# Kernel optimization log

Hardware: AMD Instinct MI355X
Metric: run time of the kernel (lower is better)

Reference implementation:

```python
import jax, jax.numpy as jnp
import numpy as np

B, S, D, H, DM, SS, A, HID = 2048, 64, 6, 4, 64, 150, 7, 256
FF = 4 * DM
DH = DM // H

def layernorm(x, g, b, eps=1e-5):
    m = jnp.mean(x, axis=-1, keepdims=True)
    v = jnp.mean((x - m) ** 2, axis=-1, keepdims=True)
    return (x - m) * jax.lax.rsqrt(v + eps) * g + b

def setup_inputs() -> dict:
    key = jax.random.key(0)
    ks = jax.random.split(key, 24)
    w = lambda k, sh: jax.random.normal(k, sh, dtype=jnp.float32) * 0.05
    inp = {
        'observation': jax.random.normal(ks[0], (B, SS), dtype=jnp.float32),
        'sequence': jax.random.normal(ks[1], (S, B, SS), dtype=jnp.float32),
        'memory': jax.random.normal(ks[2], (D, B, S, DM), dtype=jnp.float32) * 0.1,
        'length': jax.random.randint(ks[3], (1, B, 1), 0, S, dtype=jnp.int32),
        # input LayerNorm (state_size=150)
        'ln_g': jnp.ones((SS,), jnp.float32), 'ln_b': jnp.zeros((SS,), jnp.float32),
        # token_embedding replaced by Identity in source; embedding_dim(150)->dim(64) projection
        'W_emb': w(ks[4], (SS, DM)),
        # per-layer transformer params (stacked over depth)
        'ln1_g': jnp.ones((D, DM), jnp.float32), 'ln1_b': jnp.zeros((D, DM), jnp.float32),
        'ln2_g': jnp.ones((D, DM), jnp.float32), 'ln2_b': jnp.zeros((D, DM), jnp.float32),
        'Wq': w(ks[5], (D, DM, DM)), 'Wk': w(ks[6], (D, DM, DM)),
        'Wv': w(ks[7], (D, DM, DM)), 'Wo': w(ks[8], (D, DM, DM)),
        'W1': w(ks[9], (D, DM, FF)), 'b1': jnp.zeros((D, FF), jnp.float32),
        'W2': w(ks[10], (D, FF, DM)), 'b2': jnp.zeros((D, DM), jnp.float32),
        # policy MLP: dim -> 256 -> 2*action_size
        'Wp1': w(ks[11], (DM, HID)), 'bp1': jnp.zeros((HID,), jnp.float32),
        'Wp2': w(ks[12], (HID, 2 * A)), 'bp2': jnp.zeros((2 * A,), jnp.float32),
    }
    return inp

def reference(observation, sequence, memory, ln_g, ln_b, W_emb,
              ln1_g, ln1_b, ln2_g, ln2_b, Wq, Wk, Wv, Wo, W1, b1, W2, b2,
              Wp1, bp1, Wp2, bp2, length):
    # sample_forward (T == 1)
    obs = layernorm(observation, ln_g, ln_b)                      # (B,150)
    lidx = jnp.clip(length[0, :, 0], 0, S - 1)                    # (B,)
    bidx = jnp.arange(B)
    # index_put_: scatter current obs into sequence buffer at per-batch position
    seq = sequence.at[lidx, bidx].set(obs)                        # (S,B,150)
    x = jnp.einsum('bse,ed->bsd', seq.transpose(1, 0, 2), W_emb)  # (B,S,DM)
    # queries attend fully to the memory segment, causally within current segment
    causal = jnp.tril(jnp.ones((S, S), bool))
    mask = jnp.concatenate([jnp.ones((S, S), bool), causal], axis=1)  # (S, 2S)
    scale = 1.0 / np.sqrt(DH)
    new_mems = []
    for l in range(D):
        new_mems.append(x)                                        # hidden entering layer -> new memory
        h = layernorm(x, ln1_g[l], ln1_b[l])
        kv_in = jnp.concatenate([memory[l], h], axis=1)           # (B,2S,DM)
        q = (h @ Wq[l]).reshape(B, S, H, DH)
        k = (kv_in @ Wk[l]).reshape(B, 2 * S, H, DH)
        v = (kv_in @ Wv[l]).reshape(B, 2 * S, H, DH)
        scores = jnp.einsum('bqhd,bkhd->bhqk', q, k) * scale      # (B,H,S,2S)
        scores = jnp.where(mask[None, None], scores, jnp.finfo(scores.dtype).min)
        attn = jax.nn.softmax(scores, axis=-1)
        out = jnp.einsum('bhqk,bkhd->bqhd', attn, v).reshape(B, S, DM)
        x = x + out @ Wo[l]
        h2 = layernorm(x, ln2_g[l], ln2_b[l])
        x = x + jax.nn.relu(h2 @ W1[l] + b1[l]) @ W2[l] + b2[l]
    new_memory = jnp.stack(new_mems)                              # (D,B,S,DM)
    out_sb = x.transpose(1, 0, 2)                                 # (S,B,DM)
    output = out_sb[lidx, bidx]                                   # gather by length -> (B,DM)
    new_length = jnp.mod(length + 1, S)                           # (1,B,1)
    reset = (new_length[0, :, 0] == 0).astype(memory.dtype)[None, :, None, None]
    mem_out = reset * new_memory + (1.0 - reset) * memory         # masked memory reset/blend
    # policy head
    pol = jax.nn.relu(output @ Wp1 + bp1) @ Wp2 + bp2             # (B, 2A)
    std = jax.nn.softplus(pol[:, :A])
    mu = jnp.tanh(pol[:, A:])
    return (mu, std, seq, mem_out, new_length)
```

## Files before the change

kernel.cpp:

```cpp
#include <hip/hip_runtime.h>
#include <hip/hip_bf16.h>
#include <math.h>

#define NB 2048

#define LD4(p) (*(const float4*)(p))

#define O_STD 14336
#define O_SEQ 28672
#define O_MEM 19689472
#define O_LEN 70021120

#define WQT 0
#define WKT 24576
#define WVT 49152
#define WOT 73728
#define W1T 98304
#define W2T 196608
#define WET 294912

typedef __attribute__((ext_vector_type(8))) short short8v;
typedef __attribute__((ext_vector_type(4))) float f32x4;

#define MFMA(a, b, c) __builtin_amdgcn_mfma_f32_16x16x32_bf16((a), (b), (c), 0, 0, 0)

#define QSC 0.36067376022224087f

__device__ __forceinline__ short f2bf(float f) {
    return __builtin_bit_cast(short, (__bf16)f);
}
__device__ __forceinline__ unsigned pk2(float lo, float hi) {
    union { __hip_bfloat162 h; unsigned u; } t;
    t.h = __float22bfloat162_rn(make_float2(lo, hi));
    return t.u;
}

__global__ __launch_bounds__(256) void prep_weights(
        const float* __restrict__ Wq, const float* __restrict__ Wk,
        const float* __restrict__ Wv, const float* __restrict__ Wo,
        const float* __restrict__ W1, const float* __restrict__ W2,
        const float* __restrict__ Wemb, short* __restrict__ wsb) {
    int idx = blockIdx.x * 256 + threadIdx.x;
    {
        int l = idx >> 14, r = idx & 16383;
        { int n = r >> 6, k = r & 63;
          wsb[W1T + idx] = f2bf(W1[l * 16384 + k * 256 + n]); }
        { int n = r >> 8, k = r & 255;
          wsb[W2T + idx] = f2bf(W2[l * 16384 + k * 64 + n]); }
    }
    if (idx < 24576) {
        int l = idx >> 12, r = idx & 4095;
        int n = r >> 6, k = r & 63;
        int s = l * 4096 + k * 64 + n;
        wsb[WQT + idx] = f2bf(Wq[s]);
        wsb[WKT + idx] = f2bf(Wk[s]);
        wsb[WVT + idx] = f2bf(Wv[s]);
        wsb[WOT + idx] = f2bf(Wo[s]);
    }
    if (idx < 10240) {
        int n = idx / 160, k = idx - n * 160;
        wsb[WET + idx] = (k < 150) ? f2bf(Wemb[k * 64 + n]) : (short)0;
    }
}

__global__ __launch_bounds__(256) void copy4_kernel(const float4* __restrict__ src,
                                                    float4* __restrict__ dst, int n) {
    int i = blockIdx.x * 256 + threadIdx.x;
    if (i < n) dst[i] = src[i];
}

__global__ __launch_bounds__(256) void obs_ln_kernel(const float* __restrict__ obs,
        const float* __restrict__ g, const float* __restrict__ be,
        const int* __restrict__ len, float* __restrict__ outSeq, float* __restrict__ outLen) {
    int w = threadIdx.x >> 6, lane = threadIdx.x & 63;
    int b = blockIdx.x * 4 + w;
    const float* row = obs + (size_t)b * 150;
    float v0 = row[lane], v1 = row[64 + lane];
    float v2 = (lane < 22) ? row[128 + lane] : 0.f;
    float s = v0 + v1 + v2;
    #pragma unroll
    for (int m = 1; m <= 32; m <<= 1) s += __shfl_xor(s, m);
    float mean = s * (1.0f / 150.0f);
    float d0 = v0 - mean, d1 = v1 - mean;
    float d2 = (lane < 22) ? (v2 - mean) : 0.f;
    float q = d0 * d0 + d1 * d1 + d2 * d2;
    #pragma unroll
    for (int m = 1; m <= 32; m <<= 1) q += __shfl_xor(q, m);
    float rs = rsqrtf(q * (1.0f / 150.0f) + 1e-5f);
    int lenraw = len[b];
    int lidx = min(max(lenraw, 0), 63);
    float* orow = outSeq + ((size_t)lidx * NB + b) * 150;
    orow[lane]      = d0 * rs * g[lane] + be[lane];
    orow[64 + lane] = d1 * rs * g[64 + lane] + be[64 + lane];
    if (lane < 22) orow[128 + lane] = d2 * rs * g[128 + lane] + be[128 + lane];
    if (lane == 0) outLen[b] = (float)((lenraw + 1) & 63);
}

__global__ __launch_bounds__(256, 2) void mega_kernel(
        const float* __restrict__ seq, const float* __restrict__ memory,
        const int* __restrict__ len,
        const float* __restrict__ ln1g, const float* __restrict__ ln1b,
        const float* __restrict__ ln2g, const float* __restrict__ ln2b,
        const float* __restrict__ b1, const float* __restrict__ b2,
        const short* __restrict__ wsb,
        float* __restrict__ memOut, float* __restrict__ xrow) {
    __shared__ short L[20480];
    __shared__ float fls[576];
    float* lnp = fls;
    float* b1f = fls + 256;
    float* b2f = fls + 512;

    const int tid = threadIdx.x;
    const int b = blockIdx.x;
    const int w = tid >> 6;
    const int lane = tid & 63;
    const int g = lane >> 4;
    const int r16 = lane & 15;

    const int lenraw = len[b];
    const int lidx = min(max(lenraw, 0), 63);
    const bool reset = (((lenraw + 1) & 63) == 0);

    const int cxa = (r16 & 7) << 3;
    const int fc0 = (8 * g) ^ cxa;
    const int fc1 = (32 + 8 * g) ^ cxa;
    const int cxw = (g & 1) << 5;
    const int cxm = ((tid >> 2) & 7) << 3;

    const short8v zs = {0, 0, 0, 0, 0, 0, 0, 0};
    const f32x4 zf = {0.f, 0.f, 0.f, 0.f};

    #pragma unroll 1
    for (int j = 0; j < 16; ++j) {
        int r = w * 16 + j;
        int rb = r * 160;
        const float* srow = seq + ((size_t)r * NB + b) * 150;
        L[rb + lane]      = f2bf(srow[lane]);
        L[rb + 64 + lane] = f2bf(srow[64 + lane]);
        if (lane < 22)      L[rb + 128 + lane] = f2bf(srow[128 + lane]);
        else if (lane < 32) L[rb + 128 + lane] = 0;
    }
    {
        const int4* s4p = (const int4*)(wsb + WET);
        int4* d4p = (int4*)(L + 10240);
        #pragma unroll
        for (int i = 0; i < 5; ++i) d4p[tid + i * 256] = s4p[tid + i * 256];
    }
    __syncthreads();

    f32x4 x[4] = {zf, zf, zf, zf};
    #pragma unroll
    for (int kk = 0; kk < 5; ++kk) {
        short8v a = *(const short8v*)&L[(16 * w + r16) * 160 + kk * 32 + 8 * g];
        #pragma unroll
        for (int ct = 0; ct < 4; ++ct) {
            short8v bb = *(const short8v*)&L[10240 + (16 * ct + r16) * 160 + kk * 32 + 8 * g];
            x[ct] = MFMA(a, bb, x[ct]);
        }
    }
    __syncthreads();

    #pragma unroll 1
    for (int l = 0; l < 6; ++l) {
        if (tid < 64) {
            lnp[tid]       = ln1g[l * 64 + tid];
            lnp[64 + tid]  = ln1b[l * 64 + tid];
            lnp[128 + tid] = ln2g[l * 64 + tid];
            lnp[192 + tid] = ln2b[l * 64 + tid];
            b2f[tid]       = b2[l * 64 + tid];
        }
        b1f[tid] = b1[l * 256 + tid];
        {
            const float* gmem = memory + ((size_t)l * NB + b) * 4096;
            float* gout = memOut + ((size_t)l * NB + b) * 4096;
            int rr = tid >> 2, c0 = (tid & 3) * 16;
            #pragma unroll
            for (int k4 = 0; k4 < 4; ++k4) {
                float4 v = LD4(&gmem[rr * 64 + c0 + k4 * 4]);
                if (!reset) *(float4*)&gout[rr * 64 + c0 + k4 * 4] = v;
                uint2 su;
                su.x = pk2(v.x, v.y); su.y = pk2(v.z, v.w);
                *(uint2*)&L[rr * 64 + ((c0 + k4 * 4) ^ cxm)] = su;
            }
            if (reset) {
                #pragma unroll
                for (int ct = 0; ct < 4; ++ct)
                    #pragma unroll
                    for (int j = 0; j < 4; ++j)
                        gout[(16 * w + 4 * g + j) * 64 + 16 * ct + r16] = x[ct][j];
            }
        }
        {
            const int4* sq = (const int4*)(wsb + WQT + l * 4096);
            const int4* sk = (const int4*)(wsb + WKT + l * 4096);
            const int4* sv = (const int4*)(wsb + WVT + l * 4096);
            int4* dq = (int4*)(L + 8192);
            int4* dk = (int4*)(L + 12288);
            int4* dv = (int4*)(L + 16384);
            #pragma unroll
            for (int i = 0; i < 2; ++i) {
                int idx = tid + i * 256;
                int sx = idx ^ ((idx >> 3) & 7);
                dq[sx] = sq[idx];
                dk[sx] = sk[idx];
                dv[sx] = sv[idx];
            }
        }
        __syncthreads();

        #pragma unroll
        for (int j = 0; j < 4; ++j) {
            float s = x[0][j] + x[1][j] + x[2][j] + x[3][j];
            s += __shfl_xor(s, 1); s += __shfl_xor(s, 2);
            s += __shfl_xor(s, 4); s += __shfl_xor(s, 8);
            float m = s * 0.015625f;
            float q = 0.f;
            #pragma unroll
            for (int ct = 0; ct < 4; ++ct) { float d = x[ct][j] - m; q += d * d; }
            q += __shfl_xor(q, 1); q += __shfl_xor(q, 2);
            q += __shfl_xor(q, 4); q += __shfl_xor(q, 8);
            float rs = rsqrtf(q * 0.015625f + 1e-5f);
            #pragma unroll
            for (int ct = 0; ct < 4; ++ct) {
                int col = 16 * ct + r16;
                float hv = (x[ct][j] - m) * rs * lnp[col] + lnp[64 + col];
                L[(64 + 16 * w + 4 * g + j) * 64 + (col ^ (cxw | (j << 3)))] = f2bf(hv);
            }
        }
        __syncthreads();

        f32x4 qa[4] = {zf, zf, zf, zf};
        f32x4 ka[2][4] = {{zf, zf, zf, zf}, {zf, zf, zf, zf}};
        #pragma unroll
        for (int kk = 0; kk < 2; ++kk) {
            const int fc = kk ? fc1 : fc0;
            short8v ah = *(const short8v*)&L[(64 + 16 * w + r16) * 64 + fc];
            short8v a0 = *(const short8v*)&L[(16 * w + r16) * 64 + fc];
            #pragma unroll
            for (int ct = 0; ct < 4; ++ct) {
                short8v bq = *(const short8v*)&L[8192  + (16 * ct + r16) * 64 + fc];
                short8v bk = *(const short8v*)&L[12288 + (16 * ct + r16) * 64 + fc];
                qa[ct]    = MFMA(ah, bq, qa[ct]);
                ka[0][ct] = MFMA(a0, bk, ka[0][ct]);
                ka[1][ct] = MFMA(ah, bk, ka[1][ct]);
            }
        }
        __syncthreads();

        #pragma unroll
        for (int ct = 0; ct < 4; ++ct)
            #pragma unroll
            for (int j = 0; j < 4; ++j)
                L[8192 + (16 * w + 4 * g + j) * 64 + ((16 * ct + r16) ^ (cxw | (j << 3)))] =
                    f2bf(qa[ct][j] * QSC);

        f32x4 va[2][4] = {{zf, zf, zf, zf}, {zf, zf, zf, zf}};
        #pragma unroll
        for (int kk = 0; kk < 2; ++kk) {
            const int fc = kk ? fc1 : fc0;
            short8v ah = *(const short8v*)&L[(64 + 16 * w + r16) * 64 + fc];
            short8v a0 = *(const short8v*)&L[(16 * w + r16) * 64 + fc];
            #pragma unroll
            for (int ct = 0; ct < 4; ++ct) {
                short8v bv = *(const short8v*)&L[16384 + (16 * ct + r16) * 64 + fc];
                va[0][ct] = MFMA(a0, bv, va[0][ct]);
                va[1][ct] = MFMA(ah, bv, va[1][ct]);
            }
        }
        __syncthreads();

        #pragma unroll
        for (int ct = 0; ct < 4; ++ct) {
            #pragma unroll
            for (int j = 0; j < 4; ++j) {
                int key0 = 16 * w + 4 * g + j;
                int colw = (16 * ct + r16) ^ (cxw | (j << 3));
                L[key0 * 64 + colw] = f2bf(ka[0][ct][j]);
                L[(64 + key0) * 64 + colw] = f2bf(ka[1][ct][j]);
            }
        }
        {
            const int p0 = ((w >> 1) << 5) | (g << 3) | ((w & 1) << 2);
            const int p1 = p0 | 64;
            #pragma unroll
            for (int ct = 0; ct < 4; ++ct) {
                int rowb = 12288 + (16 * ct + r16) * 128;
                uint2 v0, v1;
                v0.x = pk2(va[0][ct][0], va[0][ct][1]);
                v0.y = pk2(va[0][ct][2], va[0][ct][3]);
                v1.x = pk2(va[1][ct][0], va[1][ct][1]);
                v1.y = pk2(va[1][ct][2], va[1][ct][3]);
                *(uint2*)&L[rowb + (p0 ^ cxa)] = v0;
                *(uint2*)&L[rowb + (p1 ^ cxa)] = v1;
            }
        }
        __syncthreads();

        const int hc = 16 * w;
        const int attc = (hc + 8 * g) ^ cxa;
        const int obc  = (hc + 4 * g) ^ cxa;
        #pragma unroll
        for (int qt = 0; qt < 4; ++qt) {
            const int KT = 5 + qt;
            short8v bQ = (g < 2) ? *(const short8v*)&L[8192 + (16 * qt + r16) * 64 + attc] : zs;
            f32x4 s[8];
            #pragma unroll
            for (int kt = 0; kt < 8; ++kt) if (kt < KT) {
                short8v aK = *(const short8v*)&L[(16 * kt + r16) * 64 + attc];
                s[kt] = MFMA(aK, bQ, zf);
            }
            float sum = 0.f;
            #pragma unroll
            for (int kt = 0; kt < 8; ++kt) if (kt < KT) {
                #pragma unroll
                for (int j = 0; j < 4; ++j) {
                    float e = exp2f(s[kt][j]);
                    if (kt == KT - 1) e = ((4 * g + j) > r16) ? 0.f : e;
                    s[kt][j] = e; sum += e;
                }
            }
            sum += __shfl_xor(sum, 16);
            sum += __shfl_xor(sum, 32);
            float inv = 1.0f / sum;
            f32x4 of = zf;
            const int KT2 = (KT + 1) >> 1;
            #pragma unroll
            for (int kt2 = 0; kt2 < 4; ++kt2) if (kt2 < KT2) {
                short8v aV = *(const short8v*)&L[12288 + (hc + r16) * 128 +
                                                 ((32 * kt2 + 8 * g) ^ cxa)];
                union { short8v v; unsigned u[4]; } pb;
                const int i0 = 2 * kt2, i1 = 2 * kt2 + 1;
                pb.u[0] = pk2(s[i0][0], s[i0][1]);
                pb.u[1] = pk2(s[i0][2], s[i0][3]);
                pb.u[2] = (i1 < KT) ? pk2(s[i1][0], s[i1][1]) : 0u;
                pb.u[3] = (i1 < KT) ? pk2(s[i1][2], s[i1][3]) : 0u;
                of = MFMA(aV, pb.v, of);
            }
            uint2 ov;
            ov.x = pk2(of[0] * inv, of[1] * inv);
            ov.y = pk2(of[2] * inv, of[3] * inv);
            *(uint2*)&L[8192 + (16 * qt + r16) * 64 + obc] = ov;
        }
        __syncthreads();

        {
            const int4* s = (const int4*)(wsb + WOT + l * 4096);
            int4* d = (int4*)(L + 0);
            #pragma unroll
            for (int i = 0; i < 2; ++i) {
                int idx = tid + i * 256;
                d[idx ^ ((idx >> 3) & 7)] = s[idx];
            }
        }
        __syncthreads();

        #pragma unroll
        for (int kk = 0; kk < 2; ++kk) {
            const int fc = kk ? fc1 : fc0;
            short8v a = *(const short8v*)&L[8192 + (16 * w + r16) * 64 + fc];
            #pragma unroll
            for (int ct = 0; ct < 4; ++ct) {
                short8v bb = *(const short8v*)&L[(16 * ct + r16) * 64 + fc];
                x[ct] = MFMA(a, bb, x[ct]);
            }
        }
        #pragma unroll
        for (int j = 0; j < 4; ++j) {
            float s = x[0][j] + x[1][j] + x[2][j] + x[3][j];
            s += __shfl_xor(s, 1); s += __shfl_xor(s, 2);
            s += __shfl_xor(s, 4); s += __shfl_xor(s, 8);
            float m = s * 0.015625f;
            float q = 0.f;
            #pragma unroll
            for (int ct = 0; ct < 4; ++ct) { float d = x[ct][j] - m; q += d * d; }
            q += __shfl_xor(q, 1); q += __shfl_xor(q, 2);
            q += __shfl_xor(q, 4); q += __shfl_xor(q, 8);
            float rs = rsqrtf(q * 0.015625f + 1e-5f);
            #pragma unroll
            for (int ct = 0; ct < 4; ++ct) {
                int col = 16 * ct + r16;
                float hv = (x[ct][j] - m) * rs * lnp[128 + col] + lnp[192 + col];
                L[4096 + (16 * w + 4 * g + j) * 64 + (col ^ (cxw | (j << 3)))] = f2bf(hv);
            }
        }
        __syncthreads();

        #pragma unroll 1
        for (int kb = 0; kb < 4; ++kb) {
            {
                const int4* s1 = (const int4*)(wsb + W1T + l * 16384 + kb * 4096);
                int4* d1 = (int4*)(L + 12288);
                int4* d2 = (int4*)(L + 8192);
                #pragma unroll
                for (int i = 0; i < 2; ++i) {
                    int idx = tid + i * 256;
                    int sx = idx ^ ((idx >> 3) & 7);
                    d1[sx] = s1[idx];
                    int n = idx >> 3, c = idx & 7;
                    d2[sx] = *(const int4*)&wsb[W2T + l * 16384 + n * 256 + kb * 64 + c * 8];
                }
            }
            __syncthreads();
            f32x4 tacc[4] = {zf, zf, zf, zf};
            #pragma unroll
            for (int kk = 0; kk < 2; ++kk) {
                const int fc = kk ? fc1 : fc0;
                short8v a = *(const short8v*)&L[4096 + (16 * w + r16) * 64 + fc];
                #pragma unroll
                for (int ct = 0; ct < 4; ++ct) {
                    short8v bb = *(const short8v*)&L[12288 + (16 * ct + r16) * 64 + fc];
                    tacc[ct] = MFMA(a, bb, tacc[ct]);
                }
            }
            #pragma unroll
            for (int ct = 0; ct < 4; ++ct)
                #pragma unroll
                for (int j = 0; j < 4; ++j) {
                    float v = fmaxf(tacc[ct][j] + b1f[kb * 64 + 16 * ct + r16], 0.f);
                    L[16384 + (16 * w + 4 * g + j) * 64 + ((16 * ct + r16) ^ (cxw | (j << 3)))] = f2bf(v);
                }
            __syncthreads();
            #pragma unroll
            for (int kk = 0; kk < 2; ++kk) {
                const int fc = kk ? fc1 : fc0;
                short8v a = *(const short8v*)&L[16384 + (16 * w + r16) * 64 + fc];
                #pragma unroll
                for (int ct = 0; ct < 4; ++ct) {
                    short8v bb = *(const short8v*)&L[8192 + (16 * ct + r16) * 64 + fc];
                    x[ct] = MFMA(a, bb, x[ct]);
                }
            }
            __syncthreads();
        }
        #pragma unroll
        for (int ct = 0; ct < 4; ++ct)
            #pragma unroll
            for (int j = 0; j < 4; ++j) x[ct][j] += b2f[16 * ct + r16];
    }

    if (w == (lidx >> 4) && g == ((lidx >> 2) & 3)) {
        int j = lidx & 3;
        #pragma unroll
        for (int ct = 0; ct < 4; ++ct) {
            float v = (j == 0) ? x[ct][0] : (j == 1) ? x[ct][1] : (j == 2) ? x[ct][2] : x[ct][3];
            xrow[(size_t)b * 64 + 16 * ct + r16] = v;
        }
    }
}

__device__ __forceinline__ float softplusf(float v) {
    return fmaxf(v, 0.f) + log1pf(expf(-fabsf(v)));
}

__global__ __launch_bounds__(256) void policy_kernel(const float* __restrict__ xrow,
        const float* __restrict__ Wp1, const float* __restrict__ bp1,
        const float* __restrict__ Wp2, const float* __restrict__ bp2,
        float* __restrict__ outMu, float* __restrict__ outStd) {
    __shared__ float sx[64];
    __shared__ float sh1[256];
    const int tid = threadIdx.x;
    for (int bi = 0; bi < 16; ++bi) {
        int b = blockIdx.x * 16 + bi;
        if (tid < 64) sx[tid] = xrow[(size_t)b * 64 + tid];
        __syncthreads();
        float acc = bp1[tid];
        #pragma unroll 16
        for (int k = 0; k < 64; ++k) acc = fmaf(sx[k], Wp1[k * 256 + tid], acc);
        sh1[tid] = fmaxf(acc, 0.f);
        __syncthreads();
        if (tid < 224) {
            int j = tid >> 4, gg = tid & 15;
            float a = 0.f;
            #pragma unroll
            for (int kk = 0; kk < 16; ++kk) {
                int k = gg * 16 + kk;
                a = fmaf(sh1[k], Wp2[k * 14 + j], a);
            }
            a += __shfl_xor(a, 1); a += __shfl_xor(a, 2);
            a += __shfl_xor(a, 4); a += __shfl_xor(a, 8);
            if (gg == 0) {
                float pol = a + bp2[j];
                if (j < 7) outStd[(size_t)b * 7 + j] = softplusf(pol);
                else       outMu[(size_t)b * 7 + (j - 7)] = tanhf(pol);
            }
        }
        __syncthreads();
    }
}

extern "C" void kernel_launch(void* const* d_in, const int* in_sizes, int n_in,
                              void* d_out, int out_size, void* d_ws, size_t ws_size,
                              hipStream_t stream) {
    const float* obs   = (const float*)d_in[0];
    const float* seqIn = (const float*)d_in[1];
    const float* mem   = (const float*)d_in[2];
    const int*   len   = (const int*)d_in[3];
    const float* ln_g  = (const float*)d_in[4];
    const float* ln_b  = (const float*)d_in[5];
    const float* Wemb  = (const float*)d_in[6];
    const float* ln1g  = (const float*)d_in[7];
    const float* ln1b  = (const float*)d_in[8];
    const float* ln2g  = (const float*)d_in[9];
    const float* ln2b  = (const float*)d_in[10];
    const float* Wq    = (const float*)d_in[11];
    const float* Wk    = (const float*)d_in[12];
    const float* Wv    = (const float*)d_in[13];
    const float* Wo    = (const float*)d_in[14];
    const float* W1    = (const float*)d_in[15];
    const float* b1    = (const float*)d_in[16];
    const float* W2    = (const float*)d_in[17];
    const float* b2    = (const float*)d_in[18];
    const float* Wp1   = (const float*)d_in[19];
    const float* bp1   = (const float*)d_in[20];
    const float* Wp2   = (const float*)d_in[21];
    const float* bp2   = (const float*)d_in[22];

    float* out    = (float*)d_out;
    float* outMu  = out;
    float* outStd = out + O_STD;
    float* outSeq = out + O_SEQ;
    float* outMem = out + O_MEM;
    float* outLen = out + O_LEN;
    float* xrow   = (float*)d_ws;
    short* wsb    = (short*)((char*)d_ws + 524288);

    hipLaunchKernelGGL(prep_weights, dim3(384), dim3(256), 0, stream,
                       Wq, Wk, Wv, Wo, W1, W2, Wemb, wsb);
    hipLaunchKernelGGL(copy4_kernel, dim3(19200), dim3(256), 0, stream,
                       (const float4*)seqIn, (float4*)outSeq, 4915200);
    hipLaunchKernelGGL(obs_ln_kernel, dim3(512), dim3(256), 0, stream,
                       obs, ln_g, ln_b, len, outSeq, outLen);
    hipLaunchKernelGGL(mega_kernel, dim3(2048), dim3(256), 0, stream,
                       outSeq, mem, len, ln1g, ln1b, ln2g, ln2b, b1, b2,
                       wsb, outMem, xrow);
    hipLaunchKernelGGL(policy_kernel, dim3(128), dim3(256), 0, stream,
                       xrow, Wp1, bp1, Wp2, bp2, outMu, outStd);
}
```

Baseline: 521.0 us.

## Re-plan LDS regions to prefetch Wo/W1/W2 and double-buffer FFN weight tiles

```diff
diff --git a/kernel.cpp b/kernel.cpp
--- a/kernel.cpp
+++ b/kernel.cpp
@@ -25,6 +25,14 @@
 #define MFMA(a, b, c) __builtin_amdgcn_mfma_f32_16x16x32_bf16((a), (b), (c), 0, 0, 0)
 
 #define QSC 0.36067376022224087f
+
+#define R_SKV   0
+#define R_A1    8192
+#define R_VT    12288
+#define R_WO    20480
+#define R_H2    24576
+#define R_W2B0  28672
+#define R_W2B1  32768
 
 __device__ __forceinline__ short f2bf(float f) {
     return __builtin_bit_cast(short, (__bf16)f);
@@ -104,7 +112,7 @@
         const float* __restrict__ b1, const float* __restrict__ b2,
         const short* __restrict__ wsb,
         float* __restrict__ memOut, float* __restrict__ xrow) {
-    __shared__ short L[20480];
+    __shared__ short L[36864];
     __shared__ float fls[576];
     float* lnp = fls;
     float* b1f = fls + 256;
@@ -162,6 +170,26 @@
 
     #pragma unroll 1
     for (int l = 0; l < 6; ++l) {
+        auto stage_sq = [&](const short* src, int dstbase) {
+            const int4* s = (const int4*)src;
+            int4* d = (int4*)(L + dstbase);
+            #pragma unroll
+            for (int i = 0; i < 2; ++i) {
+                int idx = tid + i * 256;
+                d[idx ^ ((idx >> 3) & 7)] = s[idx];
+            }
+        };
+        auto stage_w2 = [&](int kb, int dstbase) {
+            int4* d = (int4*)(L + dstbase);
+            #pragma unroll
+            for (int i = 0; i < 2; ++i) {
+                int idx = tid + i * 256;
+                int sx = idx ^ ((idx >> 3) & 7);
+                int n = idx >> 3, c = idx & 7;
+                d[sx] = *(const int4*)&wsb[W2T + l * 16384 + n * 256 + kb * 64 + c * 8];
+            }
+        };
+
         if (tid < 64) {
             lnp[tid]       = ln1g[l * 64 + tid];
             lnp[64 + tid]  = ln1b[l * 64 + tid];
@@ -190,22 +218,12 @@
                         gout[(16 * w + 4 * g + j) * 64 + 16 * ct + r16] = x[ct][j];
             }
         }
-        {
-            const int4* sq = (const int4*)(wsb + WQT + l * 4096);
-            const int4* sk = (const int4*)(wsb + WKT + l * 4096);
-            const int4* sv = (const int4*)(wsb + WVT + l * 4096);
-            int4* dq = (int4*)(L + 8192);
-            int4* dk = (int4*)(L + 12288);
-            int4* dv = (int4*)(L + 16384);
-            #pragma unroll
-            for (int i = 0; i < 2; ++i) {
-                int idx = tid + i * 256;
-                int sx = idx ^ ((idx >> 3) & 7);
-                dq[sx] = sq[idx];
-                dk[sx] = sk[idx];
-                dv[sx] = sv[idx];
-            }
-        }
+        stage_sq(wsb + WQT + l * 4096, R_A1);
+        stage_sq(wsb + WKT + l * 4096, R_VT);
+        stage_sq(wsb + WVT + l * 4096, R_VT + 4096);
+        stage_sq(wsb + WOT + l * 4096, R_WO);
+        stage_w2(0, R_W2B0);
+        stage_w2(1, R_W2B1);
         __syncthreads();
 
         #pragma unroll
@@ -238,8 +256,8 @@
             short8v a0 = *(const short8v*)&L[(16 * w + r16) * 64 + fc];
             #pragma unroll
             for (int ct = 0; ct < 4; ++ct) {
-                short8v bq = *(const short8v*)&L[8192  + (16 * ct + r16) * 64 + fc];
-                short8v bk = *(const short8v*)&L[12288 + (16 * ct + r16) * 64 + fc];
+                short8v bq = *(const short8v*)&L[R_A1 + (16 * ct + r16) * 64 + fc];
+                short8v bk = *(const short8v*)&L[R_VT + (16 * ct + r16) * 64 + fc];
                 qa[ct]    = MFMA(ah, bq, qa[ct]);
                 ka[0][ct] = MFMA(a0, bk, ka[0][ct]);
                 ka[1][ct] = MFMA(ah, bk, ka[1][ct]);
@@ -251,7 +269,7 @@
         for (int ct = 0; ct < 4; ++ct)
             #pragma unroll
             for (int j = 0; j < 4; ++j)
-                L[8192 + (16 * w + 4 * g + j) * 64 + ((16 * ct + r16) ^ (cxw | (j << 3)))] =
+                L[R_A1 + (16 * w + 4 * g + j) * 64 + ((16 * ct + r16) ^ (cxw | (j << 3)))] =
                     f2bf(qa[ct][j] * QSC);
 
         f32x4 va[2][4] = {{zf, zf, zf, zf}, {zf, zf, zf, zf}};
@@ -262,7 +280,7 @@
             short8v a0 = *(const short8v*)&L[(16 * w + r16) * 64 + fc];
             #pragma unroll
             for (int ct = 0; ct < 4; ++ct) {
-                short8v bv = *(const short8v*)&L[16384 + (16 * ct + r16) * 64 + fc];
+                short8v bv = *(const short8v*)&L[R_VT + 4096 + (16 * ct + r16) * 64 + fc];
                 va[0][ct] = MFMA(a0, bv, va[0][ct]);
                 va[1][ct] = MFMA(ah, bv, va[1][ct]);
             }
@@ -284,7 +302,7 @@
             const int p1 = p0 | 64;
             #pragma unroll
             for (int ct = 0; ct < 4; ++ct) {
-                int rowb = 12288 + (16 * ct + r16) * 128;
+                int rowb = R_VT + (16 * ct + r16) * 128;
                 uint2 v0, v1;
                 v0.x = pk2(va[0][ct][0], va[0][ct][1]);
                 v0.y = pk2(va[0][ct][2], va[0][ct][3]);
@@ -302,7 +320,7 @@
         #pragma unroll
         for (int qt = 0; qt < 4; ++qt) {
             const int KT = 5 + qt;
-            short8v bQ = (g < 2) ? *(const short8v*)&L[8192 + (16 * qt + r16) * 64 + attc] : zs;
+            short8v bQ = (g < 2) ? *(const short8v*)&L[R_A1 + (16 * qt + r16) * 64 + attc] : zs;
             f32x4 s[8];
             #pragma unroll
             for (int kt = 0; kt < 8; ++kt) if (kt < KT) {
@@ -326,7 +344,7 @@
             const int KT2 = (KT + 1) >> 1;
             #pragma unroll
             for (int kt2 = 0; kt2 < 4; ++kt2) if (kt2 < KT2) {
-                short8v aV = *(const short8v*)&L[12288 + (hc + r16) * 128 +
+                short8v aV = *(const short8v*)&L[R_VT + (hc + r16) * 128 +
                                                  ((32 * kt2 + 8 * g) ^ cxa)];
                 union { short8v v; unsigned u[4]; } pb;
                 const int i0 = 2 * kt2, i1 = 2 * kt2 + 1;
@@ -339,28 +357,20 @@
             uint2 ov;
             ov.x = pk2(of[0] * inv, of[1] * inv);
             ov.y = pk2(of[2] * inv, of[3] * inv);
-            *(uint2*)&L[8192 + (16 * qt + r16) * 64 + obc] = ov;
-        }
-        __syncthreads();
-
-        {
-            const int4* s = (const int4*)(wsb + WOT + l * 4096);
-            int4* d = (int4*)(L + 0);
-            #pragma unroll
-            for (int i = 0; i < 2; ++i) {
-                int idx = tid + i * 256;
-                d[idx ^ ((idx >> 3) & 7)] = s[idx];
-            }
-        }
-        __syncthreads();
+            *(uint2*)&L[R_A1 + (16 * qt + r16) * 64 + obc] = ov;
+        }
+        __syncthreads();
+
+        stage_sq(wsb + W1T + l * 16384, R_SKV);
+        stage_sq(wsb + W1T + l * 16384 + 4096, R_SKV + 4096);
 
         #pragma unroll
         for (int kk = 0; kk < 2; ++kk) {
             const int fc = kk ? fc1 : fc0;
-            short8v a = *(const short8v*)&L[8192 + (16 * w + r16) * 64 + fc];
+            short8v a = *(const short8v*)&L[R_A1 + (16 * w + r16) * 64 + fc];
             #pragma unroll
             for (int ct = 0; ct < 4; ++ct) {
-                short8v bb = *(const short8v*)&L[(16 * ct + r16) * 64 + fc];
+                short8v bb = *(const short8v*)&L[R_WO + (16 * ct + r16) * 64 + fc];
                 x[ct] = MFMA(a, bb, x[ct]);
             }
         }
@@ -380,35 +390,19 @@
             for (int ct = 0; ct < 4; ++ct) {
                 int col = 16 * ct + r16;
                 float hv = (x[ct][j] - m) * rs * lnp[128 + col] + lnp[192 + col];
-                L[4096 + (16 * w + 4 * g + j) * 64 + (col ^ (cxw | (j << 3)))] = f2bf(hv);
-            }
-        }
-        __syncthreads();
-
-        #pragma unroll 1
-        for (int kb = 0; kb < 4; ++kb) {
-            {
-                const int4* s1 = (const int4*)(wsb + W1T + l * 16384 + kb * 4096);
-                int4* d1 = (int4*)(L + 12288);
-                int4* d2 = (int4*)(L + 8192);
-                #pragma unroll
-                for (int i = 0; i < 2; ++i) {
-                    int idx = tid + i * 256;
-                    int sx = idx ^ ((idx >> 3) & 7);
-                    d1[sx] = s1[idx];
-                    int n = idx >> 3, c = idx & 7;
-                    d2[sx] = *(const int4*)&wsb[W2T + l * 16384 + n * 256 + kb * 64 + c * 8];
-                }
-            }
-            __syncthreads();
+                L[R_H2 + (16 * w + 4 * g + j) * 64 + (col ^ (cxw | (j << 3)))] = f2bf(hv);
+            }
+        }
+
+        auto ff_step = [&](int w1b, int w2b, int kb) {
             f32x4 tacc[4] = {zf, zf, zf, zf};
             #pragma unroll
             for (int kk = 0; kk < 2; ++kk) {
                 const int fc = kk ? fc1 : fc0;
-                short8v a = *(const short8v*)&L[4096 + (16 * w + r16) * 64 + fc];
+                short8v a = *(const short8v*)&L[R_H2 + (16 * w + r16) * 64 + fc];
                 #pragma unroll
                 for (int ct = 0; ct < 4; ++ct) {
-                    short8v bb = *(const short8v*)&L[12288 + (16 * ct + r16) * 64 + fc];
+                    short8v bb = *(const short8v*)&L[w1b + (16 * ct + r16) * 64 + fc];
                     tacc[ct] = MFMA(a, bb, tacc[ct]);
                 }
             }
@@ -417,25 +411,37 @@
                 #pragma unroll
                 for (int j = 0; j < 4; ++j) {
                     float v = fmaxf(tacc[ct][j] + b1f[kb * 64 + 16 * ct + r16], 0.f);
-                    L[16384 + (16 * w + 4 * g + j) * 64 + ((16 * ct + r16) ^ (cxw | (j << 3)))] = f2bf(v);
+                    L[R_A1 + (16 * w + 4 * g + j) * 64 + ((16 * ct + r16) ^ (cxw | (j << 3)))] = f2bf(v);
                 }
-            __syncthreads();
             #pragma unroll
             for (int kk = 0; kk < 2; ++kk) {
                 const int fc = kk ? fc1 : fc0;
-                short8v a = *(const short8v*)&L[16384 + (16 * w + r16) * 64 + fc];
+                short8v a = *(const short8v*)&L[R_A1 + (16 * w + r16) * 64 + fc];
                 #pragma unroll
                 for (int ct = 0; ct < 4; ++ct) {
-                    short8v bb = *(const short8v*)&L[8192 + (16 * ct + r16) * 64 + fc];
+                    short8v bb = *(const short8v*)&L[w2b + (16 * ct + r16) * 64 + fc];
                     x[ct] = MFMA(a, bb, x[ct]);
                 }
             }
-            __syncthreads();
-        }
+        };
+
+        __syncthreads();
+        ff_step(R_SKV, R_W2B0, 0);
+        __syncthreads();
+        stage_sq(wsb + W1T + l * 16384 + 2 * 4096, R_SKV);
+        stage_w2(2, R_W2B0);
+        ff_step(R_SKV + 4096, R_W2B1, 1);
+        __syncthreads();
+        stage_sq(wsb + W1T + l * 16384 + 3 * 4096, R_SKV + 4096);
+        stage_w2(3, R_W2B1);
+        ff_step(R_SKV, R_W2B0, 2);
+        __syncthreads();
+        ff_step(R_SKV + 4096, R_W2B1, 3);
         #pragma unroll
         for (int ct = 0; ct < 4; ++ct)
             #pragma unroll
             for (int j = 0; j < 4; ++j) x[ct][j] += b2f[16 * ct + r16];
+        __syncthreads();
     }
 
     if (w == (lidx >> 4) && g == ((lidx >> 2) & 3)) {
```

Measured after the change: 497.5 us (median of 2 runs). -4.5%, faster.
